# Kernel tuning notes

Hardware: AMD Instinct MI355X
Metric: run time of the kernel (lower is better)

## Reference

```python
import jax, jax.numpy as jnp
import numpy as np

B, S, DM, H = 4, 4096, 1024, 16
HD = DM // H  # 64


def setup_inputs() -> dict:
    key = jax.random.key(0)
    ks = jax.random.split(key, 9)
    sc = 0.02
    x = jax.random.normal(ks[0], (B, S, DM), dtype=jnp.float32)
    Wq = jax.random.normal(ks[1], (DM, DM), dtype=jnp.float32) * sc
    bq = jnp.zeros((DM,), dtype=jnp.float32)
    Wk = jax.random.normal(ks[2], (DM, HD), dtype=jnp.float32) * sc
    bk = jnp.zeros((HD,), dtype=jnp.float32)
    Wv = jax.random.normal(ks[3], (DM, HD), dtype=jnp.float32) * sc
    bv = jnp.zeros((HD,), dtype=jnp.float32)
    Wo = jax.random.normal(ks[4], (DM, DM), dtype=jnp.float32) * sc
    bo = jnp.zeros((DM,), dtype=jnp.float32)
    return {"x": x, "Wq": Wq, "bq": bq, "Wk": Wk, "bk": bk,
            "Wv": Wv, "bv": bv, "Wo": Wo, "bo": bo}


def reference(x, Wq, bq, Wk, bk, Wv, bv, Wo, bo):
    b, s, _ = x.shape
    q = (x @ Wq + bq).reshape(b, s, H, HD)          # [B,S,H,D]
    k = (x @ Wk + bk)                                # [B,S,D] (single KV head)
    v = (x @ Wv + bv)                                # [B,S,D]
    # Faithful to source: k/v expanded over head axis, matmul over last two
    # dims of [B,S,H,D] -> scores are per-token head-vs-head: [B,S,H,H].
    k_e = jnp.broadcast_to(k[:, :, None, :], (b, s, H, HD))
    v_e = jnp.broadcast_to(v[:, :, None, :], (b, s, H, HD))
    scores = jnp.einsum('bshd,bsgd->bshg', q, k_e) / jnp.sqrt(jnp.float32(HD))
    attn = jax.nn.softmax(scores, axis=-1)           # uniform (scores const over g)
    out = jnp.einsum('bshg,bsgd->bshd', attn, v_e)   # [B,S,H,D]
    return out.reshape(b, s, DM) @ Wo + bo
```

## Files before the change

### kernel.cpp

```cpp
#include <hip/hip_runtime.h>

#define M_TOTAL 16384
#define DMODEL  1024
#define HDIM    64
#define NHEAD   16

typedef _Float16 half8 __attribute__((ext_vector_type(8)));
typedef float    f32x4 __attribute__((ext_vector_type(4)));
typedef float    f32x2 __attribute__((ext_vector_type(2)));

__global__ __launch_bounds__(256) void prep_kernel(const float* __restrict__ Wv,
                                                   const float* __restrict__ Wo,
                                                   _Float16* __restrict__ WvT,
                                                   _Float16* __restrict__ WosumT) {
    const int t = blockIdx.x * 256 + threadIdx.x;
    {
        const int d = t & 63, k = t >> 6;
        WvT[d * DMODEL + k] = (_Float16)Wv[k * HDIM + d];
    }
    {
        const int n = t & 1023, d = t >> 10;
        float s = 0.f;
        #pragma unroll
        for (int h = 0; h < NHEAD; ++h) s += Wo[(h * HDIM + d) * DMODEL + n];
        WosumT[n * HDIM + d] = (_Float16)s;
    }
}

#define VP_S 68

__global__ __launch_bounds__(512, 4) void vproj_kernel(const float* __restrict__ X,
                                                       const float* __restrict__ bv,
                                                       const _Float16* __restrict__ WvT,
                                                       _Float16* __restrict__ V) {
    __shared__ float Vp[8][16][VP_S];

    const int tid = threadIdx.x;
    const int l   = tid & 63;
    const int w   = tid >> 6;
    const int lr  = l & 15;
    const int lk  = l >> 4;
    const int m0  = blockIdx.x * 16;
    const int k0  = w * 128;

    const float* xp = X + (size_t)(m0 + lr) * DMODEL + k0 + lk * 8;
    f32x4 xb[8];
    #pragma unroll
    for (int s = 0; s < 4; ++s) {
        xb[2 * s]     = *(const f32x4*)(xp + s * 32);
        xb[2 * s + 1] = *(const f32x4*)(xp + s * 32 + 4);
    }
    half8 Bf[4][4];
    #pragma unroll
    for (int n4 = 0; n4 < 4; ++n4)
        #pragma unroll
        for (int s = 0; s < 4; ++s)
            Bf[n4][s] = *(const half8*)&WvT[(size_t)(n4 * 16 + lr) * DMODEL + k0 + s * 32 + lk * 8];

    f32x4 acc[4] = {};
    #pragma unroll
    for (int s = 0; s < 4; ++s) {
        union { _Float16 h[8]; half8 v; } pk;
        #pragma unroll
        for (int j = 0; j < 4; ++j) {
            pk.h[j]     = (_Float16)xb[2 * s][j];
            pk.h[4 + j] = (_Float16)xb[2 * s + 1][j];
        }
        #pragma unroll
        for (int n4 = 0; n4 < 4; ++n4)
            acc[n4] = __builtin_amdgcn_mfma_f32_16x16x32_f16(pk.v, Bf[n4][s], acc[n4], 0, 0, 0);
    }
    #pragma unroll
    for (int n4 = 0; n4 < 4; ++n4)
        #pragma unroll
        for (int j = 0; j < 4; ++j)
            Vp[w][lk * 4 + j][n4 * 16 + lr] = acc[n4][j];
    __syncthreads();

    const int idx = tid * 2;
    const int r   = idx >> 6;
    const int c   = idx & 63;
    f32x2 s2 = {};
    #pragma unroll
    for (int p = 0; p < 8; ++p) s2 += *(const f32x2*)&Vp[p][r][c];
    s2 += *(const f32x2*)&bv[c];
    union { _Float16 h[2]; unsigned int u; } o;
    o.h[0] = (_Float16)s2[0];
    o.h[1] = (_Float16)s2[1];
    *(unsigned int*)&V[(size_t)(m0 + r) * HDIM + c] = o.u;
}

__global__ __launch_bounds__(256) void oproj_kernel(const _Float16* __restrict__ V,
                                                    const float* __restrict__ bo,
                                                    const _Float16* __restrict__ WosumT,
                                                    float* __restrict__ Out) {
    const int tid = threadIdx.x;
    const int l   = tid & 63;
    const int w   = tid >> 6;
    const int lr  = l & 15;
    const int lk  = l >> 4;
    const int m0  = blockIdx.x * 16;

    const _Float16* vp = V + (size_t)(m0 + lr) * HDIM + lk * 8;
    const half8 a0 = *(const half8*)vp;
    const half8 a1 = *(const half8*)(vp + 32);

    #pragma unroll 4
    for (int nf = 0; nf < 16; ++nf) {
        const int n0 = w * 256 + nf * 16;
        const half8 b0 = *(const half8*)&WosumT[(size_t)(n0 + lr) * HDIM + lk * 8];
        const half8 b1 = *(const half8*)&WosumT[(size_t)(n0 + lr) * HDIM + 32 + lk * 8];
        f32x4 o = {};
        o = __builtin_amdgcn_mfma_f32_16x16x32_f16(a0, b0, o, 0, 0, 0);
        o = __builtin_amdgcn_mfma_f32_16x16x32_f16(a1, b1, o, 0, 0, 0);
        const float bov = bo[n0 + lr];
        #pragma unroll
        for (int j = 0; j < 4; ++j)
            Out[(size_t)(m0 + lk * 4 + j) * DMODEL + n0 + lr] = o[j] + bov;
    }
}

extern "C" void kernel_launch(void* const* d_in, const int* in_sizes, int n_in,
                              void* d_out, int out_size, void* d_ws, size_t ws_size,
                              hipStream_t stream) {
    const float* x  = (const float*)d_in[0];
    const float* Wv = (const float*)d_in[5];
    const float* bv = (const float*)d_in[6];
    const float* Wo = (const float*)d_in[7];
    const float* bo = (const float*)d_in[8];

    _Float16* WvT    = (_Float16*)d_ws;
    _Float16* WosumT = (_Float16*)((char*)d_ws + 64 * 1024 * 2);
    _Float16* V      = (_Float16*)((char*)d_ws + 256 * 1024);
    float*    out    = (float*)d_out;

    prep_kernel<<<256, 256, 0, stream>>>(Wv, Wo, WvT, WosumT);
    vproj_kernel<<<M_TOTAL / 16, 512, 0, stream>>>(x, bv, WvT, V);
    oproj_kernel<<<M_TOTAL / 16, 256, 0, stream>>>(V, bo, WosumT, out);
}
```

Before: 56.85 us.

## Fuse V projection and output projection into one kernel via LDS

Merges the V-projection and the folded output-projection kernels into a single kernel. The per-tile V result (16 rows x 64) stays in shared memory as fp16 instead of going out to global memory and back. This removes one kernel launch and the global round trip of V. In exchange it adds a second barrier and extra LDS per block, and the 8 waves now each write 128 output columns in this one kernel.

```diff
diff --git a/kernel.cpp b/kernel.cpp
--- a/kernel.cpp
+++ b/kernel.cpp
@@ -28,12 +28,16 @@
 }
 
 #define VP_S 68
+#define VH_S 72
 
-__global__ __launch_bounds__(512, 4) void vproj_kernel(const float* __restrict__ X,
-                                                       const float* __restrict__ bv,
-                                                       const _Float16* __restrict__ WvT,
-                                                       _Float16* __restrict__ V) {
-    __shared__ float Vp[8][16][VP_S];
+__global__ __launch_bounds__(512, 4) void mqa_fused(const float* __restrict__ X,
+                                                    const float* __restrict__ bv,
+                                                    const float* __restrict__ bo,
+                                                    const _Float16* __restrict__ WvT,
+                                                    const _Float16* __restrict__ WosumT,
+                                                    float* __restrict__ Out) {
+    __shared__ float    Vp[8][16][VP_S];
+    __shared__ _Float16 Vh[16 * VH_S];
 
     const int tid = threadIdx.x;
     const int l   = tid & 63;
@@ -77,46 +81,44 @@
             Vp[w][lk * 4 + j][n4 * 16 + lr] = acc[n4][j];
     __syncthreads();
 
-    const int idx = tid * 2;
-    const int r   = idx >> 6;
-    const int c   = idx & 63;
-    f32x2 s2 = {};
+    {
+        const int idx = tid * 2;
+        const int r   = idx >> 6;
+        const int c   = idx & 63;
+        f32x2 s2 = {};
+        #pragma unroll
+        for (int p = 0; p < 8; ++p) s2 += *(const f32x2*)&Vp[p][r][c];
+        s2 += *(const f32x2*)&bv[c];
+        union { _Float16 h[2]; unsigned int u; } o;
+        o.h[0] = (_Float16)s2[0];
+        o.h[1] = (_Float16)s2[1];
+        *(unsigned int*)&Vh[r * VH_S + c] = o.u;
+    }
+    __syncthreads();
+
+    const half8 a0 = *(const half8*)&Vh[lr * VH_S + lk * 8];
+    const half8 a1 = *(const half8*)&Vh[lr * VH_S + 32 + lk * 8];
+
     #pragma unroll
-    for (int p = 0; p < 8; ++p) s2 += *(const f32x2*)&Vp[p][r][c];
-    s2 += *(const f32x2*)&bv[c];
-    union { _Float16 h[2]; unsigned int u; } o;
-    o.h[0] = (_Float16)s2[0];
-    o.h[1] = (_Float16)s2[1];
-    *(unsigned int*)&V[(size_t)(m0 + r) * HDIM + c] = o.u;
-}
-
-__global__ __launch_bounds__(256) void oproj_kernel(const _Float16* __restrict__ V,
-                                                    const float* __restrict__ bo,
-                                                    const _Float16* __restrict__ WosumT,
-                                                    float* __restrict__ Out) {
-    const int tid = threadIdx.x;
-    const int l   = tid & 63;
-    const int w   = tid >> 6;
-    const int lr  = l & 15;
-    const int lk  = l >> 4;
-    const int m0  = blockIdx.x * 16;
-
-    const _Float16* vp = V + (size_t)(m0 + lr) * HDIM + lk * 8;
-    const half8 a0 = *(const half8*)vp;
-    const half8 a1 = *(const half8*)(vp + 32);
-
-    #pragma unroll 4
-    for (int nf = 0; nf < 16; ++nf) {
-        const int n0 = w * 256 + nf * 16;
-        const half8 b0 = *(const half8*)&WosumT[(size_t)(n0 + lr) * HDIM + lk * 8];
-        const half8 b1 = *(const half8*)&WosumT[(size_t)(n0 + lr) * HDIM + 32 + lk * 8];
-        f32x4 o = {};
-        o = __builtin_amdgcn_mfma_f32_16x16x32_f16(a0, b0, o, 0, 0, 0);
-        o = __builtin_amdgcn_mfma_f32_16x16x32_f16(a1, b1, o, 0, 0, 0);
-        const float bov = bo[n0 + lr];
+    for (int h = 0; h < 2; ++h) {
+        const int cb = w * 128 + h * 64;
+        half8 B2[4][2];
         #pragma unroll
-        for (int j = 0; j < 4; ++j)
-            Out[(size_t)(m0 + lk * 4 + j) * DMODEL + n0 + lr] = o[j] + bov;
+        for (int t = 0; t < 4; ++t) {
+            const _Float16* wb = &WosumT[(size_t)(cb + t * 16 + lr) * HDIM];
+            B2[t][0] = *(const half8*)(wb + lk * 8);
+            B2[t][1] = *(const half8*)(wb + 32 + lk * 8);
+        }
+        #pragma unroll
+        for (int t = 0; t < 4; ++t) {
+            f32x4 o = {};
+            o = __builtin_amdgcn_mfma_f32_16x16x32_f16(a0, B2[t][0], o, 0, 0, 0);
+            o = __builtin_amdgcn_mfma_f32_16x16x32_f16(a1, B2[t][1], o, 0, 0, 0);
+            const float bov = bo[cb + t * 16 + lr];
+            #pragma unroll
+            for (int j = 0; j < 4; ++j)
+                Out[(size_t)(m0 + lk * 4 + j) * DMODEL + cb + t * 16 + lr] = o[j] + bov;
+        }
     }
 }
 
@@ -131,10 +133,8 @@
 
     _Float16* WvT    = (_Float16*)d_ws;
     _Float16* WosumT = (_Float16*)((char*)d_ws + 64 * 1024 * 2);
-    _Float16* V      = (_Float16*)((char*)d_ws + 256 * 1024);
     float*    out    = (float*)d_out;
 
     prep_kernel<<<256, 256, 0, stream>>>(Wv, Wo, WvT, WosumT);
-    vproj_kernel<<<M_TOTAL / 16, 512, 0, stream>>>(x, bv, WvT, V);
-    oproj_kernel<<<M_TOTAL / 16, 256, 0, stream>>>(V, bo, WosumT, out);
+    mqa_fused<<<M_TOTAL / 16, 512, 0, stream>>>(x, bv, bo, WvT, WosumT, out);
 }
```

After: 55.48 us. 2.4% less time.
